# Kernel optimization log

Hardware: AMD Instinct MI355X
Metric: run time of the kernel (lower is better)

## Reference

```python
import jax, jax.numpy as jnp
import numpy as np

N, F, H, C, E = 100000, 128, 128, 40, 1600000


def setup_inputs() -> dict:
    key = jax.random.key(0)
    ks = jax.random.split(key, 8)
    x = jax.random.normal(ks[0], (N, F), dtype=jnp.float32)
    edge_index = jax.random.randint(ks[1], (2, E), 0, N, dtype=jnp.int64)
    s = 0.05
    return {
        "x": x,
        "edge_index": edge_index,
        "eps1": jnp.float32(0.0),
        "w1": jax.random.normal(ks[2], (F, H), dtype=jnp.float32) * s,
        "b1": jnp.zeros((H,), jnp.float32),
        "w2": jax.random.normal(ks[3], (H, H), dtype=jnp.float32) * s,
        "b2": jnp.zeros((H,), jnp.float32),
        "eps2": jnp.float32(0.0),
        "w3": jax.random.normal(ks[4], (H, H), dtype=jnp.float32) * s,
        "b3": jnp.zeros((H,), jnp.float32),
        "w4": jax.random.normal(ks[5], (H, C), dtype=jnp.float32) * s,
        "b4": jnp.zeros((C,), jnp.float32),
    }


def _gin_aggregate(h, src, dst, eps, n):
    # sum_{j -> i} h_j  +  (1+eps) * h_i
    agg = jax.ops.segment_sum(h[src], dst, num_segments=n)
    return (1.0 + eps) * h + agg


def reference(x, edge_index, eps1, w1, b1, w2, b2, eps2, w3, b3, w4, b4):
    src, dst = edge_index[0], edge_index[1]
    n = x.shape[0]
    # conv1: GINConv with MLP = Lin-ReLU-Lin-ReLU
    h = _gin_aggregate(x, src, dst, eps1, n)
    h = jax.nn.relu(h @ w1 + b1)
    h = jax.nn.relu(h @ w2 + b2)
    h = jax.nn.relu(h)  # outer F.relu (idempotent, kept for faithfulness)
    # dropout: identity in eval mode
    # conv2: GINConv with MLP = Lin-ReLU-Lin
    h2 = _gin_aggregate(h, src, dst, eps2, n)
    h2 = jax.nn.relu(h2 @ w3 + b3)
    h2 = h2 @ w4 + b4
    return jax.nn.log_softmax(h2, axis=1)
```

## Files before the change

kernel.cpp:

```cpp
#include <hip/hip_runtime.h>
#include <hip/hip_fp16.h>
#include <math.h>

constexpr int F = 128;
constexpr int C = 40;
constexpr int LDH = 136;
constexpr int BSHIFT = 8;
constexpr int BSIZE = 1 << BSHIFT;
constexpr int CHUNK = 8192;

typedef __attribute__((ext_vector_type(8))) _Float16 half8;
typedef __attribute__((ext_vector_type(4))) float float4v;


__global__ __launch_bounds__(256) void coarse_hist_kernel(const int* __restrict__ dst, int E, int NB,
                                                          int* __restrict__ coarse_count) {
    __shared__ int hist[512];
    int t = threadIdx.x;
    int c0 = blockIdx.x * CHUNK;
    int cend = min(c0 + CHUNK, E);
    for (int i = t; i < NB; i += 256) hist[i] = 0;
    __syncthreads();
    for (int i = c0 + t; i < cend; i += 256)
        atomicAdd(&hist[dst[i] >> BSHIFT], 1);
    __syncthreads();
    for (int i = t; i < NB; i += 256)
        if (hist[i]) atomicAdd(&coarse_count[i], hist[i]);
}

__global__ __launch_bounds__(512) void coarse_scan_kernel(const int* __restrict__ coarse_count,
                                                          int NB, int E,
                                                          int* __restrict__ coarse_start,
                                                          int* __restrict__ bucket_pos,
                                                          int* __restrict__ row_start, int N) {
    __shared__ int tmp[512];
    int t = threadIdx.x;
    int v = (t < NB) ? coarse_count[t] : 0;
    tmp[t] = v;
    __syncthreads();
    for (int d = 1; d < 512; d <<= 1) {
        int add = (t >= d) ? tmp[t - d] : 0;
        __syncthreads();
        tmp[t] += add;
        __syncthreads();
    }
    if (t < NB) {
        int ex = tmp[t] - v;
        coarse_start[t] = ex;
        bucket_pos[t] = ex;
    }
    if (t == 0) {
        coarse_start[NB] = E;
        row_start[N] = E;
    }
}

__global__ __launch_bounds__(256) void bucket_scatter_a_kernel(
        const int* __restrict__ src, const int* __restrict__ dst, int E, int NB,
        int* __restrict__ bucket_pos, unsigned* __restrict__ pairs) {
    __shared__ int hist[512];
    __shared__ int base[512];
    int t = threadIdx.x;
    int c0 = blockIdx.x * CHUNK;
    int cend = min(c0 + CHUNK, E);
    for (int i = t; i < NB; i += 256) hist[i] = 0;
    __syncthreads();
    for (int i = c0 + t; i < cend; i += 256)
        atomicAdd(&hist[dst[i] >> BSHIFT], 1);
    __syncthreads();
    for (int i = t; i < NB; i += 256) {
        int h = hist[i];
        base[i] = (h > 0) ? atomicAdd(&bucket_pos[i], h) : 0;
        hist[i] = 0;
    }
    __syncthreads();
    for (int i = c0 + t; i < cend; i += 256) {
        int d = dst[i];
        int b = d >> BSHIFT;
        int p = base[b] + atomicAdd(&hist[b], 1);
        pairs[p] = ((unsigned)(d & (BSIZE - 1)) << 24) | (unsigned)src[i];
    }
}

__global__ __launch_bounds__(256) void bucket_sort_kernel(const unsigned* __restrict__ pairs,
                                                          const int* __restrict__ coarse_start,
                                                          int N, int* __restrict__ row_start,
                                                          int* __restrict__ src_sorted) {
    __shared__ int hist[256];
    __shared__ int tmp[256];
    int b = blockIdx.x, t = threadIdx.x;
    int base = b << BSHIFT;
    int start = coarse_start[b];
    int end = coarse_start[b + 1];
    hist[t] = 0;
    __syncthreads();
    for (int i = start + t; i < end; i += 256)
        atomicAdd(&hist[pairs[i] >> 24], 1);
    __syncthreads();
    int v = hist[t];
    tmp[t] = v;
    __syncthreads();
    for (int d = 1; d < 256; d <<= 1) {
        int add = (t >= d) ? tmp[t - d] : 0;
        __syncthreads();
        tmp[t] += add;
        __syncthreads();
    }
    int ex = start + tmp[t] - v;
    if (base + t < N) row_start[base + t] = ex;
    hist[t] = ex;
    __syncthreads();
    for (int i = start + t; i < end; i += 256) {
        unsigned u = pairs[i];
        int p = atomicAdd(&hist[u >> 24], 1);
        src_sorted[p] = (int)(u & 0x00FFFFFFu);
    }
}


__global__ void conv_f16_kernel(const float* __restrict__ in, __half* __restrict__ out, int n4,
                                int* __restrict__ coarse_count, int NB) {
    int i = blockIdx.x * blockDim.x + threadIdx.x;
    if (blockIdx.x == 0) {
        for (int j = threadIdx.x; j < NB; j += 256) coarse_count[j] = 0;
    }
    if (i >= n4) return;
    float4 v = ((const float4*)in)[i];
    __half2 a = __floats2half2_rn(v.x, v.y);
    __half2 b = __floats2half2_rn(v.z, v.w);
    uint2 o;
    o.x = __builtin_bit_cast(unsigned, a);
    o.y = __builtin_bit_cast(unsigned, b);
    ((uint2*)out)[i] = o;
}


__global__ __launch_bounds__(256) void prep_weights_kernel(
        const float* __restrict__ w1, const float* __restrict__ w2,
        const float* __restrict__ w3, const float* __restrict__ w4,
        __half* __restrict__ w1t, __half* __restrict__ w2t,
        __half* __restrict__ w3t, __half* __restrict__ w4t) {
    __shared__ float lds[128 * 128];
    const float* in; __half* outp; int Nin, Npad;
    switch (blockIdx.x) {
        case 0:  in = w1; outp = w1t; Nin = 128; Npad = 128; break;
        case 1:  in = w2; outp = w2t; Nin = 128; Npad = 128; break;
        case 2:  in = w3; outp = w3t; Nin = 128; Npad = 128; break;
        default: in = w4; outp = w4t; Nin = 40;  Npad = 48;  break;
    }
    int t = threadIdx.x;
    int nf4 = 128 * Nin / 4;
    for (int i = t; i < nf4; i += 256)
        ((float4*)lds)[i] = ((const float4*)in)[i];
    __syncthreads();
    int total = Npad * 64;
    for (int i = t; i < total; i += 256) {
        int n = i >> 6, k2 = (i & 63) * 2;
        float lo = 0.f, hi = 0.f;
        if (n < Nin) {
            lo = lds[k2 * Nin + n];
            hi = lds[(k2 + 1) * Nin + n];
        }
        __half2 h = __floats2half2_rn(lo, hi);
        ((unsigned*)outp)[i] = __builtin_bit_cast(unsigned, h);
    }
}


__global__ __launch_bounds__(256) void agg_f16_kernel(const __half* __restrict__ feat,
        const int* __restrict__ row_start, const int* __restrict__ src_sorted,
        const float* __restrict__ eps_ptr, __half* __restrict__ out, int N) {
    int wid = (int)((blockIdx.x * blockDim.x + threadIdx.x) >> 6);
    int lane = threadIdx.x & 63;
    if (wid >= N) return;
    int q = lane >> 4, l16 = lane & 15;
    int s = row_start[wid], e = row_start[wid + 1];
    __half2 A0, A1, A2, A3, B0, B1, B2, B3;
    A0 = A1 = A2 = A3 = B0 = B1 = B2 = B3 = __builtin_bit_cast(__half2, 0u);
    int i = s + q;
    for (; i + 4 < e; i += 8) {
        int sv0 = src_sorted[i];
        int sv1 = src_sorted[i + 4];
        uint4 u0 = *(((const uint4*)(feat + (size_t)sv0 * F)) + l16);
        uint4 u1 = *(((const uint4*)(feat + (size_t)sv1 * F)) + l16);
        A0 = __hadd2(A0, __builtin_bit_cast(__half2, u0.x));
        A1 = __hadd2(A1, __builtin_bit_cast(__half2, u0.y));
        A2 = __hadd2(A2, __builtin_bit_cast(__half2, u0.z));
        A3 = __hadd2(A3, __builtin_bit_cast(__half2, u0.w));
        B0 = __hadd2(B0, __builtin_bit_cast(__half2, u1.x));
        B1 = __hadd2(B1, __builtin_bit_cast(__half2, u1.y));
        B2 = __hadd2(B2, __builtin_bit_cast(__half2, u1.z));
        B3 = __hadd2(B3, __builtin_bit_cast(__half2, u1.w));
    }
    if (i < e) {
        int sv = src_sorted[i];
        uint4 u = *(((const uint4*)(feat + (size_t)sv * F)) + l16);
        A0 = __hadd2(A0, __builtin_bit_cast(__half2, u.x));
        A1 = __hadd2(A1, __builtin_bit_cast(__half2, u.y));
        A2 = __hadd2(A2, __builtin_bit_cast(__half2, u.z));
        A3 = __hadd2(A3, __builtin_bit_cast(__half2, u.w));
    }
    float a[8];
    {
        float2 fa, fb;
        fa = __half22float2(A0); fb = __half22float2(B0); a[0] = fa.x + fb.x; a[1] = fa.y + fb.y;
        fa = __half22float2(A1); fb = __half22float2(B1); a[2] = fa.x + fb.x; a[3] = fa.y + fb.y;
        fa = __half22float2(A2); fb = __half22float2(B2); a[4] = fa.x + fb.x; a[5] = fa.y + fb.y;
        fa = __half22float2(A3); fb = __half22float2(B3); a[6] = fa.x + fb.x; a[7] = fa.y + fb.y;
    }
#pragma unroll
    for (int j = 0; j < 8; ++j) {
        a[j] += __shfl_xor(a[j], 16);
        a[j] += __shfl_xor(a[j], 32);
    }
    if (q == 0) {
        float ep1 = 1.0f + *eps_ptr;
        uint4 u = *(((const uint4*)(feat + (size_t)wid * F)) + l16);
        float2 s0 = __half22float2(__builtin_bit_cast(__half2, u.x));
        float2 s1 = __half22float2(__builtin_bit_cast(__half2, u.y));
        float2 s2 = __half22float2(__builtin_bit_cast(__half2, u.z));
        float2 s3 = __half22float2(__builtin_bit_cast(__half2, u.w));
        a[0] = fmaf(ep1, s0.x, a[0]); a[1] = fmaf(ep1, s0.y, a[1]);
        a[2] = fmaf(ep1, s1.x, a[2]); a[3] = fmaf(ep1, s1.y, a[3]);
        a[4] = fmaf(ep1, s2.x, a[4]); a[5] = fmaf(ep1, s2.y, a[5]);
        a[6] = fmaf(ep1, s3.x, a[6]); a[7] = fmaf(ep1, s3.y, a[7]);
        uint4 ou;
        ou.x = __builtin_bit_cast(unsigned, __floats2half2_rn(a[0], a[1]));
        ou.y = __builtin_bit_cast(unsigned, __floats2half2_rn(a[2], a[3]));
        ou.z = __builtin_bit_cast(unsigned, __floats2half2_rn(a[4], a[5]));
        ou.w = __builtin_bit_cast(unsigned, __floats2half2_rn(a[6], a[7]));
        *(((uint4*)(out + (size_t)wid * F)) + l16) = ou;
    }
}


__global__ __launch_bounds__(256) void mlp1_mfma_kernel(const __half* __restrict__ A,
        const __half* __restrict__ w1t, const float* __restrict__ b1,
        const __half* __restrict__ w2t, const float* __restrict__ b2,
        __half* __restrict__ out, int N) {
    __shared__ __half ldsA[64 * LDH];
    __shared__ __half ldsW[128 * LDH];
    __shared__ float ldsB[256];
    int t = threadIdx.x;
    int wave = t >> 6, lane = t & 63, quad = lane >> 4, l16 = lane & 15;
    int br = blockIdx.x * 64;
    if (t < 128) ldsB[t] = b1[t];
    else         ldsB[t] = b2[t - 128];
    for (int i = t; i < 1024; i += 256) {
        int r = i >> 4, c = i & 15;
        int gr = br + r;
        uint4 v = make_uint4(0u, 0u, 0u, 0u);
        if (gr < N) v = *((const uint4*)(A + (size_t)gr * F + c * 8));
        *((uint4*)&ldsA[r * LDH + c * 8]) = v;
    }
    for (int i = t; i < 2048; i += 256) {
        int r = i >> 4, c = i & 15;
        *((uint4*)&ldsW[r * LDH + c * 8]) = *((const uint4*)(w1t + r * 128 + c * 8));
    }
    __syncthreads();

    int ct0 = wave * 2;
    float4v acc[4][2];
    float4v zero = {0.f, 0.f, 0.f, 0.f};
#pragma unroll
    for (int i = 0; i < 4; ++i)
#pragma unroll
        for (int j = 0; j < 2; ++j) acc[i][j] = zero;

#pragma unroll
    for (int ks = 0; ks < 4; ++ks) {
        half8 af[4], wf[2];
#pragma unroll
        for (int i = 0; i < 4; ++i)
            af[i] = *((const half8*)&ldsA[(i * 16 + l16) * LDH + ks * 32 + quad * 8]);
#pragma unroll
        for (int j = 0; j < 2; ++j)
            wf[j] = *((const half8*)&ldsW[((ct0 + j) * 16 + l16) * LDH + ks * 32 + quad * 8]);
#pragma unroll
        for (int i = 0; i < 4; ++i)
#pragma unroll
            for (int j = 0; j < 2; ++j)
                acc[i][j] = __builtin_amdgcn_mfma_f32_16x16x32_f16(wf[j], af[i], acc[i][j], 0, 0, 0);
    }
    __syncthreads();
#pragma unroll
    for (int j = 0; j < 2; ++j) {
        int c = ct0 + j;
        float4 bb = *((const float4*)&ldsB[c * 16 + quad * 4]);
#pragma unroll
        for (int i = 0; i < 4; ++i) {
            float v0 = acc[i][j][0] + bb.x; v0 = v0 > 0.f ? v0 : 0.f;
            float v1 = acc[i][j][1] + bb.y; v1 = v1 > 0.f ? v1 : 0.f;
            float v2 = acc[i][j][2] + bb.z; v2 = v2 > 0.f ? v2 : 0.f;
            float v3 = acc[i][j][3] + bb.w; v3 = v3 > 0.f ? v3 : 0.f;
            __half2 h0 = __floats2half2_rn(v0, v1);
            __half2 h1 = __floats2half2_rn(v2, v3);
            uint2 o;
            o.x = __builtin_bit_cast(unsigned, h0);
            o.y = __builtin_bit_cast(unsigned, h1);
            *((uint2*)&ldsA[(i * 16 + l16) * LDH + c * 16 + quad * 4]) = o;
        }
    }
    for (int i = t; i < 2048; i += 256) {
        int r = i >> 4, c = i & 15;
        *((uint4*)&ldsW[r * LDH + c * 8]) = *((const uint4*)(w2t + r * 128 + c * 8));
    }
    __syncthreads();

#pragma unroll
    for (int i = 0; i < 4; ++i)
#pragma unroll
        for (int j = 0; j < 2; ++j) acc[i][j] = zero;
#pragma unroll
    for (int ks = 0; ks < 4; ++ks) {
        half8 af[4], wf[2];
#pragma unroll
        for (int i = 0; i < 4; ++i)
            af[i] = *((const half8*)&ldsA[(i * 16 + l16) * LDH + ks * 32 + quad * 8]);
#pragma unroll
        for (int j = 0; j < 2; ++j)
            wf[j] = *((const half8*)&ldsW[((ct0 + j) * 16 + l16) * LDH + ks * 32 + quad * 8]);
#pragma unroll
        for (int i = 0; i < 4; ++i)
#pragma unroll
            for (int j = 0; j < 2; ++j)
                acc[i][j] = __builtin_amdgcn_mfma_f32_16x16x32_f16(wf[j], af[i], acc[i][j], 0, 0, 0);
    }
    __syncthreads();
#pragma unroll
    for (int j = 0; j < 2; ++j) {
        int c = ct0 + j;
        float4 bb = *((const float4*)&ldsB[128 + c * 16 + quad * 4]);
#pragma unroll
        for (int i = 0; i < 4; ++i) {
            float v0 = acc[i][j][0] + bb.x; v0 = v0 > 0.f ? v0 : 0.f;
            float v1 = acc[i][j][1] + bb.y; v1 = v1 > 0.f ? v1 : 0.f;
            float v2 = acc[i][j][2] + bb.z; v2 = v2 > 0.f ? v2 : 0.f;
            float v3 = acc[i][j][3] + bb.w; v3 = v3 > 0.f ? v3 : 0.f;
            __half2 h0 = __floats2half2_rn(v0, v1);
            __half2 h1 = __floats2half2_rn(v2, v3);
            uint2 o;
            o.x = __builtin_bit_cast(unsigned, h0);
            o.y = __builtin_bit_cast(unsigned, h1);
            *((uint2*)&ldsA[(i * 16 + l16) * LDH + c * 16 + quad * 4]) = o;
        }
    }
    __syncthreads();
    for (int i = t; i < 1024; i += 256) {
        int r = i >> 4, c = i & 15;
        int gr = br + r;
        if (gr < N)
            *((uint4*)(out + (size_t)gr * F + c * 8)) = *((const uint4*)&ldsA[r * LDH + c * 8]);
    }
}


__global__ __launch_bounds__(256) void mlp2_mfma_kernel(const __half* __restrict__ A,
        const __half* __restrict__ w3t, const float* __restrict__ b3,
        const __half* __restrict__ w4t, const float* __restrict__ b4,
        float* __restrict__ out, int N) {
    __shared__ __half ldsA[64 * LDH];
    __shared__ __half ldsW[128 * LDH];
    __shared__ float ldsB[176];
    int t = threadIdx.x;
    int wave = t >> 6, lane = t & 63, quad = lane >> 4, l16 = lane & 15;
    int br = blockIdx.x * 64;
    if (t < 128) ldsB[t] = b3[t];
    else if (t < 176) ldsB[t] = (t - 128 < C) ? b4[t - 128] : 0.f;
    for (int i = t; i < 1024; i += 256) {
        int r = i >> 4, c = i & 15;
        int gr = br + r;
        uint4 v = make_uint4(0u, 0u, 0u, 0u);
        if (gr < N) v = *((const uint4*)(A + (size_t)gr * F + c * 8));
        *((uint4*)&ldsA[r * LDH + c * 8]) = v;
    }
    for (int i = t; i < 2048; i += 256) {
        int r = i >> 4, c = i & 15;
        *((uint4*)&ldsW[r * LDH + c * 8]) = *((const uint4*)(w3t + r * 128 + c * 8));
    }
    __syncthreads();

    int ct0 = wave * 2;
    float4v acc[4][2];
    float4v zero = {0.f, 0.f, 0.f, 0.f};
#pragma unroll
    for (int i = 0; i < 4; ++i)
#pragma unroll
        for (int j = 0; j < 2; ++j) acc[i][j] = zero;
#pragma unroll
    for (int ks = 0; ks < 4; ++ks) {
        half8 af[4], wf[2];
#pragma unroll
        for (int i = 0; i < 4; ++i)
            af[i] = *((const half8*)&ldsA[(i * 16 + l16) * LDH + ks * 32 + quad * 8]);
#pragma unroll
        for (int j = 0; j < 2; ++j)
            wf[j] = *((const half8*)&ldsW[((ct0 + j) * 16 + l16) * LDH + ks * 32 + quad * 8]);
#pragma unroll
        for (int i = 0; i < 4; ++i)
#pragma unroll
            for (int j = 0; j < 2; ++j)
                acc[i][j] = __builtin_amdgcn_mfma_f32_16x16x32_f16(wf[j], af[i], acc[i][j], 0, 0, 0);
    }
    __syncthreads();
#pragma unroll
    for (int j = 0; j < 2; ++j) {
        int c = ct0 + j;
        float4 bb = *((const float4*)&ldsB[c * 16 + quad * 4]);
#pragma unroll
        for (int i = 0; i < 4; ++i) {
            float v0 = acc[i][j][0] + bb.x; v0 = v0 > 0.f ? v0 : 0.f;
            float v1 = acc[i][j][1] + bb.y; v1 = v1 > 0.f ? v1 : 0.f;
            float v2 = acc[i][j][2] + bb.z; v2 = v2 > 0.f ? v2 : 0.f;
            float v3 = acc[i][j][3] + bb.w; v3 = v3 > 0.f ? v3 : 0.f;
            __half2 h0 = __floats2half2_rn(v0, v1);
            __half2 h1 = __floats2half2_rn(v2, v3);
            uint2 o;
            o.x = __builtin_bit_cast(unsigned, h0);
            o.y = __builtin_bit_cast(unsigned, h1);
            *((uint2*)&ldsA[(i * 16 + l16) * LDH + c * 16 + quad * 4]) = o;
        }
    }
    for (int i = t; i < 768; i += 256) {
        int r = i >> 4, c = i & 15;
        *((uint4*)&ldsW[r * LDH + c * 8]) = *((const uint4*)(w4t + r * 128 + c * 8));
    }
    __syncthreads();

    float4v acc4[3];
#pragma unroll
    for (int c = 0; c < 3; ++c) acc4[c] = zero;
#pragma unroll
    for (int ks = 0; ks < 4; ++ks) {
        half8 af = *((const half8*)&ldsA[(wave * 16 + l16) * LDH + ks * 32 + quad * 8]);
#pragma unroll
        for (int c = 0; c < 3; ++c) {
            half8 wf = *((const half8*)&ldsW[(c * 16 + l16) * LDH + ks * 32 + quad * 8]);
            acc4[c] = __builtin_amdgcn_mfma_f32_16x16x32_f16(wf, af, acc4[c], 0, 0, 0);
        }
    }
    float lv[3][4];
#pragma unroll
    for (int c = 0; c < 3; ++c) {
        float4 bb = *((const float4*)&ldsB[128 + c * 16 + quad * 4]);
        lv[c][0] = acc4[c][0] + bb.x;
        lv[c][1] = acc4[c][1] + bb.y;
        lv[c][2] = acc4[c][2] + bb.z;
        lv[c][3] = acc4[c][3] + bb.w;
    }
    bool tile2ok = (quad < 2);
    float m = -1e30f;
#pragma unroll
    for (int c = 0; c < 3; ++c) {
        if (c == 2 && !tile2ok) continue;
#pragma unroll
        for (int r = 0; r < 4; ++r) m = fmaxf(m, lv[c][r]);
    }
    m = fmaxf(m, __shfl_xor(m, 16));
    m = fmaxf(m, __shfl_xor(m, 32));
    float ssum = 0.f;
#pragma unroll
    for (int c = 0; c < 3; ++c) {
        if (c == 2 && !tile2ok) continue;
#pragma unroll
        for (int r = 0; r < 4; ++r) ssum += __expf(lv[c][r] - m);
    }
    ssum += __shfl_xor(ssum, 16);
    ssum += __shfl_xor(ssum, 32);
    float L = m + __logf(ssum);
    int node = br + wave * 16 + l16;
    if (node < N) {
#pragma unroll
        for (int c = 0; c < 3; ++c) {
            if (c == 2 && !tile2ok) continue;
            float4 o = make_float4(lv[c][0] - L, lv[c][1] - L, lv[c][2] - L, lv[c][3] - L);
            *((float4*)(out + (size_t)node * C + c * 16 + quad * 4)) = o;
        }
    }
}


extern "C" void kernel_launch(void* const* d_in, const int* in_sizes, int n_in,
                              void* d_out, int out_size, void* d_ws, size_t ws_size,
                              hipStream_t stream) {
    const float* x    = (const float*)d_in[0];
    const int*   ei   = (const int*)d_in[1];
    const float* eps1 = (const float*)d_in[2];
    const float* w1   = (const float*)d_in[3];
    const float* b1   = (const float*)d_in[4];
    const float* w2   = (const float*)d_in[5];
    const float* b2   = (const float*)d_in[6];
    const float* eps2 = (const float*)d_in[7];
    const float* w3   = (const float*)d_in[8];
    const float* b3   = (const float*)d_in[9];
    const float* w4   = (const float*)d_in[10];
    const float* b4   = (const float*)d_in[11];
    float* out = (float*)d_out;

    int N = in_sizes[0] / F;
    int E = in_sizes[1] / 2;
    const int* src = ei;
    const int* dst = ei + E;

    int NB = (N + BSIZE - 1) >> BSHIFT;
    int BA = (E + CHUNK - 1) / CHUNK;

    __half* x_h  = (__half*)d_ws;
    __half* h0_h = x_h + (size_t)N * F;
    __half* h_h  = h0_h + (size_t)N * F;
    __half* w1t  = h_h + (size_t)N * F;
    __half* w2t  = w1t + 128 * 128;
    __half* w3t  = w2t + 128 * 128;
    __half* w4t  = w3t + 128 * 128;
    unsigned* pairs   = (unsigned*)(w4t + 48 * 128);
    int* row_start    = (int*)(pairs + E);
    int* src_sorted   = row_start + (N + 1);
    int* coarse_count = src_sorted + E;
    int* coarse_start = coarse_count + 512;
    int* bucket_pos   = coarse_start + 513;

    int n4 = N * F / 4;
    conv_f16_kernel<<<(n4 + 255) / 256, 256, 0, stream>>>(x, x_h, n4, coarse_count, NB);
    prep_weights_kernel<<<4, 256, 0, stream>>>(w1, w2, w3, w4, w1t, w2t, w3t, w4t);

    coarse_hist_kernel<<<BA, 256, 0, stream>>>(dst, E, NB, coarse_count);
    coarse_scan_kernel<<<1, 512, 0, stream>>>(coarse_count, NB, E, coarse_start, bucket_pos,
                                              row_start, N);
    bucket_scatter_a_kernel<<<BA, 256, 0, stream>>>(src, dst, E, NB, bucket_pos, pairs);
    bucket_sort_kernel<<<NB, 256, 0, stream>>>(pairs, coarse_start, N, row_start, src_sorted);

    agg_f16_kernel<<<(N + 3) / 4, 256, 0, stream>>>(x_h, row_start, src_sorted, eps1, h0_h, N);
    mlp1_mfma_kernel<<<(N + 63) / 64, 256, 0, stream>>>(h0_h, w1t, b1, w2t, b2, h_h, N);
    agg_f16_kernel<<<(N + 3) / 4, 256, 0, stream>>>(h_h, row_start, src_sorted, eps2, h0_h, N);
    mlp2_mfma_kernel<<<(N + 63) / 64, 256, 0, stream>>>(h0_h, w3t, b3, w4t, b4, out, N);
}
```

Baseline: 352.0 us.

## Fuse prep kernels and process two nodes per wave in aggregation

The histogram, weight transpose and x-to-fp16 conversion kernels are merged into one launch, and a memset now zeroes the coarse counts. The aggregation kernel now gives each wave two destination nodes, loads up to 16 neighbor indices per node in one coalesced read, spreads them with shuffles, and issues eight feature gathers per iteration. This cuts launch count and raises memory-level parallelism in the gather. In exchange it adds masked redundant loads for low-degree nodes and more register pressure, and the weight transpose now runs in four passes through a smaller LDS buffer.

New measurement: 344.4 us. -2.2%, faster.

```diff
diff --git a/kernel.cpp b/kernel.cpp
--- a/kernel.cpp
+++ b/kernel.cpp
@@ -13,20 +13,66 @@
 typedef __attribute__((ext_vector_type(4))) float float4v;
 
 
-__global__ __launch_bounds__(256) void coarse_hist_kernel(const int* __restrict__ dst, int E, int NB,
-                                                          int* __restrict__ coarse_count) {
-    __shared__ int hist[512];
-    int t = threadIdx.x;
-    int c0 = blockIdx.x * CHUNK;
-    int cend = min(c0 + CHUNK, E);
-    for (int i = t; i < NB; i += 256) hist[i] = 0;
-    __syncthreads();
-    for (int i = c0 + t; i < cend; i += 256)
-        atomicAdd(&hist[dst[i] >> BSHIFT], 1);
-    __syncthreads();
-    for (int i = t; i < NB; i += 256)
-        if (hist[i]) atomicAdd(&coarse_count[i], hist[i]);
-}
+__global__ __launch_bounds__(256) void fused_prep_kernel(
+        const float* __restrict__ x, __half* __restrict__ x_h, int n4,
+        const int* __restrict__ dst, int E, int NB, int* __restrict__ coarse_count,
+        const float* __restrict__ w1, const float* __restrict__ w2,
+        const float* __restrict__ w3, const float* __restrict__ w4,
+        __half* __restrict__ w1t, __half* __restrict__ w2t,
+        __half* __restrict__ w3t, __half* __restrict__ w4t, int BA) {
+    __shared__ float smem[4096];
+    int b = blockIdx.x, t = threadIdx.x;
+    if (b < BA) {
+        int* hist = (int*)smem;
+        int c0 = b * CHUNK, cend = min(c0 + CHUNK, E);
+        for (int i = t; i < NB; i += 256) hist[i] = 0;
+        __syncthreads();
+        for (int i = c0 + t; i < cend; i += 256)
+            atomicAdd(&hist[dst[i] >> BSHIFT], 1);
+        __syncthreads();
+        for (int i = t; i < NB; i += 256)
+            if (hist[i]) atomicAdd(&coarse_count[i], hist[i]);
+        return;
+    }
+    if (b < BA + 4) {
+        const float* in; __half* outp; int Nin, Npad;
+        switch (b - BA) {
+            case 0:  in = w1; outp = w1t; Nin = 128; Npad = 128; break;
+            case 1:  in = w2; outp = w2t; Nin = 128; Npad = 128; break;
+            case 2:  in = w3; outp = w3t; Nin = 128; Npad = 128; break;
+            default: in = w4; outp = w4t; Nin = 40;  Npad = 48;  break;
+        }
+        for (int p = 0; p < 4; ++p) {
+            int nf4 = 32 * Nin / 4;
+            const float4* srcv = (const float4*)(in + 32 * p * Nin);
+            for (int i = t; i < nf4; i += 256) ((float4*)smem)[i] = srcv[i];
+            __syncthreads();
+            int total = Npad * 16;
+            for (int i = t; i < total; i += 256) {
+                int n = i >> 4, wl = i & 15;
+                float lo = 0.f, hi = 0.f;
+                if (n < Nin) {
+                    lo = smem[(2 * wl) * Nin + n];
+                    hi = smem[(2 * wl + 1) * Nin + n];
+                }
+                __half2 h = __floats2half2_rn(lo, hi);
+                ((unsigned*)outp)[n * 64 + 16 * p + wl] = __builtin_bit_cast(unsigned, h);
+            }
+            __syncthreads();
+        }
+        return;
+    }
+    int i = (b - BA - 4) * 256 + t;
+    if (i >= n4) return;
+    float4 v = ((const float4*)x)[i];
+    __half2 a = __floats2half2_rn(v.x, v.y);
+    __half2 bb = __floats2half2_rn(v.z, v.w);
+    uint2 o;
+    o.x = __builtin_bit_cast(unsigned, a);
+    o.y = __builtin_bit_cast(unsigned, bb);
+    ((uint2*)x_h)[i] = o;
+}
+
 
 __global__ __launch_bounds__(512) void coarse_scan_kernel(const int* __restrict__ coarse_count,
                                                           int NB, int E,
@@ -118,118 +164,140 @@
 }
 
 
-__global__ void conv_f16_kernel(const float* __restrict__ in, __half* __restrict__ out, int n4,
-                                int* __restrict__ coarse_count, int NB) {
-    int i = blockIdx.x * blockDim.x + threadIdx.x;
-    if (blockIdx.x == 0) {
-        for (int j = threadIdx.x; j < NB; j += 256) coarse_count[j] = 0;
-    }
-    if (i >= n4) return;
-    float4 v = ((const float4*)in)[i];
-    __half2 a = __floats2half2_rn(v.x, v.y);
-    __half2 b = __floats2half2_rn(v.z, v.w);
-    uint2 o;
-    o.x = __builtin_bit_cast(unsigned, a);
-    o.y = __builtin_bit_cast(unsigned, b);
-    ((uint2*)out)[i] = o;
-}
-
-
-__global__ __launch_bounds__(256) void prep_weights_kernel(
-        const float* __restrict__ w1, const float* __restrict__ w2,
-        const float* __restrict__ w3, const float* __restrict__ w4,
-        __half* __restrict__ w1t, __half* __restrict__ w2t,
-        __half* __restrict__ w3t, __half* __restrict__ w4t) {
-    __shared__ float lds[128 * 128];
-    const float* in; __half* outp; int Nin, Npad;
-    switch (blockIdx.x) {
-        case 0:  in = w1; outp = w1t; Nin = 128; Npad = 128; break;
-        case 1:  in = w2; outp = w2t; Nin = 128; Npad = 128; break;
-        case 2:  in = w3; outp = w3t; Nin = 128; Npad = 128; break;
-        default: in = w4; outp = w4t; Nin = 40;  Npad = 48;  break;
-    }
-    int t = threadIdx.x;
-    int nf4 = 128 * Nin / 4;
-    for (int i = t; i < nf4; i += 256)
-        ((float4*)lds)[i] = ((const float4*)in)[i];
-    __syncthreads();
-    int total = Npad * 64;
-    for (int i = t; i < total; i += 256) {
-        int n = i >> 6, k2 = (i & 63) * 2;
-        float lo = 0.f, hi = 0.f;
-        if (n < Nin) {
-            lo = lds[k2 * Nin + n];
-            hi = lds[(k2 + 1) * Nin + n];
-        }
-        __half2 h = __floats2half2_rn(lo, hi);
-        ((unsigned*)outp)[i] = __builtin_bit_cast(unsigned, h);
-    }
-}
-
-
 __global__ __launch_bounds__(256) void agg_f16_kernel(const __half* __restrict__ feat,
         const int* __restrict__ row_start, const int* __restrict__ src_sorted,
         const float* __restrict__ eps_ptr, __half* __restrict__ out, int N) {
-    int wid = (int)((blockIdx.x * blockDim.x + threadIdx.x) >> 6);
+    int wp = (int)((blockIdx.x * blockDim.x + threadIdx.x) >> 6);
     int lane = threadIdx.x & 63;
-    if (wid >= N) return;
+    int n0 = wp * 2;
+    if (n0 >= N) return;
     int q = lane >> 4, l16 = lane & 15;
-    int s = row_start[wid], e = row_start[wid + 1];
-    __half2 A0, A1, A2, A3, B0, B1, B2, B3;
-    A0 = A1 = A2 = A3 = B0 = B1 = B2 = B3 = __builtin_bit_cast(__half2, 0u);
-    int i = s + q;
-    for (; i + 4 < e; i += 8) {
-        int sv0 = src_sorted[i];
-        int sv1 = src_sorted[i + 4];
-        uint4 u0 = *(((const uint4*)(feat + (size_t)sv0 * F)) + l16);
-        uint4 u1 = *(((const uint4*)(feat + (size_t)sv1 * F)) + l16);
-        A0 = __hadd2(A0, __builtin_bit_cast(__half2, u0.x));
-        A1 = __hadd2(A1, __builtin_bit_cast(__half2, u0.y));
-        A2 = __hadd2(A2, __builtin_bit_cast(__half2, u0.z));
-        A3 = __hadd2(A3, __builtin_bit_cast(__half2, u0.w));
-        B0 = __hadd2(B0, __builtin_bit_cast(__half2, u1.x));
-        B1 = __hadd2(B1, __builtin_bit_cast(__half2, u1.y));
-        B2 = __hadd2(B2, __builtin_bit_cast(__half2, u1.z));
-        B3 = __hadd2(B3, __builtin_bit_cast(__half2, u1.w));
-    }
-    if (i < e) {
-        int sv = src_sorted[i];
-        uint4 u = *(((const uint4*)(feat + (size_t)sv * F)) + l16);
-        A0 = __hadd2(A0, __builtin_bit_cast(__half2, u.x));
-        A1 = __hadd2(A1, __builtin_bit_cast(__half2, u.y));
-        A2 = __hadd2(A2, __builtin_bit_cast(__half2, u.z));
-        A3 = __hadd2(A3, __builtin_bit_cast(__half2, u.w));
-    }
-    float a[8];
+    bool has1 = (n0 + 1) < N;
+    int s0 = row_start[n0];
+    int e0 = row_start[n0 + 1];
+    int s1 = e0;
+    int e1 = has1 ? row_start[n0 + 2] : e0;
+    uint4 self0 = *(((const uint4*)(feat + (size_t)n0 * F)) + l16);
+    uint4 self1 = has1 ? *(((const uint4*)(feat + (size_t)(n0 + 1) * F)) + l16)
+                       : make_uint4(0u, 0u, 0u, 0u);
+    float ep1 = 1.0f + *eps_ptr;
+    __half2 PA0, PA1, PA2, PA3, PB0, PB1, PB2, PB3;
+    __half2 QA0, QA1, QA2, QA3, QB0, QB1, QB2, QB3;
+    PA0 = PA1 = PA2 = PA3 = PB0 = PB1 = PB2 = PB3 = __builtin_bit_cast(__half2, 0u);
+    QA0 = QA1 = QA2 = QA3 = QB0 = QB1 = QB2 = QB3 = __builtin_bit_cast(__half2, 0u);
+    const uint4 z4 = make_uint4(0u, 0u, 0u, 0u);
+    int i0 = s0, i1 = s1;
+    while (i0 < e0 || i1 < e1) {
+        int svA = src_sorted[max(min(i0 + l16, e0 - 1), 0)];
+        int svB = src_sorted[max(min(i1 + l16, e1 - 1), 0)];
+        int a0 = __shfl(svA, q);
+        int a1 = __shfl(svA, q + 4);
+        int a2 = __shfl(svA, q + 8);
+        int a3 = __shfl(svA, q + 12);
+        int b0 = __shfl(svB, q);
+        int b1 = __shfl(svB, q + 4);
+        int b2 = __shfl(svB, q + 8);
+        int b3 = __shfl(svB, q + 12);
+        uint4 uA0 = *(((const uint4*)(feat + (size_t)a0 * F)) + l16);
+        uint4 uA1 = *(((const uint4*)(feat + (size_t)a1 * F)) + l16);
+        uint4 uA2 = *(((const uint4*)(feat + (size_t)a2 * F)) + l16);
+        uint4 uA3 = *(((const uint4*)(feat + (size_t)a3 * F)) + l16);
+        uint4 uB0 = *(((const uint4*)(feat + (size_t)b0 * F)) + l16);
+        uint4 uB1 = *(((const uint4*)(feat + (size_t)b1 * F)) + l16);
+        uint4 uB2 = *(((const uint4*)(feat + (size_t)b2 * F)) + l16);
+        uint4 uB3 = *(((const uint4*)(feat + (size_t)b3 * F)) + l16);
+        if (i0 + q >= e0)      uA0 = z4;
+        if (i0 + q + 4 >= e0)  uA1 = z4;
+        if (i0 + q + 8 >= e0)  uA2 = z4;
+        if (i0 + q + 12 >= e0) uA3 = z4;
+        if (i1 + q >= e1)      uB0 = z4;
+        if (i1 + q + 4 >= e1)  uB1 = z4;
+        if (i1 + q + 8 >= e1)  uB2 = z4;
+        if (i1 + q + 12 >= e1) uB3 = z4;
+        PA0 = __hadd2(PA0, __builtin_bit_cast(__half2, uA0.x));
+        PA1 = __hadd2(PA1, __builtin_bit_cast(__half2, uA0.y));
+        PA2 = __hadd2(PA2, __builtin_bit_cast(__half2, uA0.z));
+        PA3 = __hadd2(PA3, __builtin_bit_cast(__half2, uA0.w));
+        PB0 = __hadd2(PB0, __builtin_bit_cast(__half2, uA1.x));
+        PB1 = __hadd2(PB1, __builtin_bit_cast(__half2, uA1.y));
+        PB2 = __hadd2(PB2, __builtin_bit_cast(__half2, uA1.z));
+        PB3 = __hadd2(PB3, __builtin_bit_cast(__half2, uA1.w));
+        PA0 = __hadd2(PA0, __builtin_bit_cast(__half2, uA2.x));
+        PA1 = __hadd2(PA1, __builtin_bit_cast(__half2, uA2.y));
+        PA2 = __hadd2(PA2, __builtin_bit_cast(__half2, uA2.z));
+        PA3 = __hadd2(PA3, __builtin_bit_cast(__half2, uA2.w));
+        PB0 = __hadd2(PB0, __builtin_bit_cast(__half2, uA3.x));
+        PB1 = __hadd2(PB1, __builtin_bit_cast(__half2, uA3.y));
+        PB2 = __hadd2(PB2, __builtin_bit_cast(__half2, uA3.z));
+        PB3 = __hadd2(PB3, __builtin_bit_cast(__half2, uA3.w));
+        QA0 = __hadd2(QA0, __builtin_bit_cast(__half2, uB0.x));
+        QA1 = __hadd2(QA1, __builtin_bit_cast(__half2, uB0.y));
+        QA2 = __hadd2(QA2, __builtin_bit_cast(__half2, uB0.z));
+        QA3 = __hadd2(QA3, __builtin_bit_cast(__half2, uB0.w));
+        QB0 = __hadd2(QB0, __builtin_bit_cast(__half2, uB1.x));
+        QB1 = __hadd2(QB1, __builtin_bit_cast(__half2, uB1.y));
+        QB2 = __hadd2(QB2, __builtin_bit_cast(__half2, uB1.z));
+        QB3 = __hadd2(QB3, __builtin_bit_cast(__half2, uB1.w));
+        QA0 = __hadd2(QA0, __builtin_bit_cast(__half2, uB2.x));
+        QA1 = __hadd2(QA1, __builtin_bit_cast(__half2, uB2.y));
+        QA2 = __hadd2(QA2, __builtin_bit_cast(__half2, uB2.z));
+        QA3 = __hadd2(QA3, __builtin_bit_cast(__half2, uB2.w));
+        QB0 = __hadd2(QB0, __builtin_bit_cast(__half2, uB3.x));
+        QB1 = __hadd2(QB1, __builtin_bit_cast(__half2, uB3.y));
+        QB2 = __hadd2(QB2, __builtin_bit_cast(__half2, uB3.z));
+        QB3 = __hadd2(QB3, __builtin_bit_cast(__half2, uB3.w));
+        i0 += 16;
+        i1 += 16;
+    }
+    float a[8], c[8];
     {
         float2 fa, fb;
-        fa = __half22float2(A0); fb = __half22float2(B0); a[0] = fa.x + fb.x; a[1] = fa.y + fb.y;
-        fa = __half22float2(A1); fb = __half22float2(B1); a[2] = fa.x + fb.x; a[3] = fa.y + fb.y;
-        fa = __half22float2(A2); fb = __half22float2(B2); a[4] = fa.x + fb.x; a[5] = fa.y + fb.y;
-        fa = __half22float2(A3); fb = __half22float2(B3); a[6] = fa.x + fb.x; a[7] = fa.y + fb.y;
+        fa = __half22float2(PA0); fb = __half22float2(PB0); a[0] = fa.x + fb.x; a[1] = fa.y + fb.y;
+        fa = __half22float2(PA1); fb = __half22float2(PB1); a[2] = fa.x + fb.x; a[3] = fa.y + fb.y;
+        fa = __half22float2(PA2); fb = __half22float2(PB2); a[4] = fa.x + fb.x; a[5] = fa.y + fb.y;
+        fa = __half22float2(PA3); fb = __half22float2(PB3); a[6] = fa.x + fb.x; a[7] = fa.y + fb.y;
+        fa = __half22float2(QA0); fb = __half22float2(QB0); c[0] = fa.x + fb.x; c[1] = fa.y + fb.y;
+        fa = __half22float2(QA1); fb = __half22float2(QB1); c[2] = fa.x + fb.x; c[3] = fa.y + fb.y;
+        fa = __half22float2(QA2); fb = __half22float2(QB2); c[4] = fa.x + fb.x; c[5] = fa.y + fb.y;
+        fa = __half22float2(QA3); fb = __half22float2(QB3); c[6] = fa.x + fb.x; c[7] = fa.y + fb.y;
     }
 #pragma unroll
     for (int j = 0; j < 8; ++j) {
         a[j] += __shfl_xor(a[j], 16);
         a[j] += __shfl_xor(a[j], 32);
+        c[j] += __shfl_xor(c[j], 16);
+        c[j] += __shfl_xor(c[j], 32);
     }
     if (q == 0) {
-        float ep1 = 1.0f + *eps_ptr;
-        uint4 u = *(((const uint4*)(feat + (size_t)wid * F)) + l16);
-        float2 s0 = __half22float2(__builtin_bit_cast(__half2, u.x));
-        float2 s1 = __half22float2(__builtin_bit_cast(__half2, u.y));
-        float2 s2 = __half22float2(__builtin_bit_cast(__half2, u.z));
-        float2 s3 = __half22float2(__builtin_bit_cast(__half2, u.w));
-        a[0] = fmaf(ep1, s0.x, a[0]); a[1] = fmaf(ep1, s0.y, a[1]);
-        a[2] = fmaf(ep1, s1.x, a[2]); a[3] = fmaf(ep1, s1.y, a[3]);
-        a[4] = fmaf(ep1, s2.x, a[4]); a[5] = fmaf(ep1, s2.y, a[5]);
-        a[6] = fmaf(ep1, s3.x, a[6]); a[7] = fmaf(ep1, s3.y, a[7]);
+        float2 s0f = __half22float2(__builtin_bit_cast(__half2, self0.x));
+        float2 s1f = __half22float2(__builtin_bit_cast(__half2, self0.y));
+        float2 s2f = __half22float2(__builtin_bit_cast(__half2, self0.z));
+        float2 s3f = __half22float2(__builtin_bit_cast(__half2, self0.w));
+        a[0] = fmaf(ep1, s0f.x, a[0]); a[1] = fmaf(ep1, s0f.y, a[1]);
+        a[2] = fmaf(ep1, s1f.x, a[2]); a[3] = fmaf(ep1, s1f.y, a[3]);
+        a[4] = fmaf(ep1, s2f.x, a[4]); a[5] = fmaf(ep1, s2f.y, a[5]);
+        a[6] = fmaf(ep1, s3f.x, a[6]); a[7] = fmaf(ep1, s3f.y, a[7]);
         uint4 ou;
         ou.x = __builtin_bit_cast(unsigned, __floats2half2_rn(a[0], a[1]));
         ou.y = __builtin_bit_cast(unsigned, __floats2half2_rn(a[2], a[3]));
         ou.z = __builtin_bit_cast(unsigned, __floats2half2_rn(a[4], a[5]));
         ou.w = __builtin_bit_cast(unsigned, __floats2half2_rn(a[6], a[7]));
-        *(((uint4*)(out + (size_t)wid * F)) + l16) = ou;
+        *(((uint4*)(out + (size_t)n0 * F)) + l16) = ou;
+    } else if (q == 1 && has1) {
+        float2 s0f = __half22float2(__builtin_bit_cast(__half2, self1.x));
+        float2 s1f = __half22float2(__builtin_bit_cast(__half2, self1.y));
+        float2 s2f = __half22float2(__builtin_bit_cast(__half2, self1.z));
+        float2 s3f = __half22float2(__builtin_bit_cast(__half2, self1.w));
+        c[0] = fmaf(ep1, s0f.x, c[0]); c[1] = fmaf(ep1, s0f.y, c[1]);
+        c[2] = fmaf(ep1, s1f.x, c[2]); c[3] = fmaf(ep1, s1f.y, c[3]);
+        c[4] = fmaf(ep1, s2f.x, c[4]); c[5] = fmaf(ep1, s2f.y, c[5]);
+        c[6] = fmaf(ep1, s3f.x, c[6]); c[7] = fmaf(ep1, s3f.y, c[7]);
+        uint4 ou;
+        ou.x = __builtin_bit_cast(unsigned, __floats2half2_rn(c[0], c[1]));
+        ou.y = __builtin_bit_cast(unsigned, __floats2half2_rn(c[2], c[3]));
+        ou.z = __builtin_bit_cast(unsigned, __floats2half2_rn(c[4], c[5]));
+        ou.w = __builtin_bit_cast(unsigned, __floats2half2_rn(c[6], c[7]));
+        *(((uint4*)(out + (size_t)(n0 + 1) * F)) + l16) = ou;
     }
 }
 
@@ -520,17 +588,21 @@
     int* bucket_pos   = coarse_start + 513;
 
     int n4 = N * F / 4;
-    conv_f16_kernel<<<(n4 + 255) / 256, 256, 0, stream>>>(x, x_h, n4, coarse_count, NB);
-    prep_weights_kernel<<<4, 256, 0, stream>>>(w1, w2, w3, w4, w1t, w2t, w3t, w4t);
-
-    coarse_hist_kernel<<<BA, 256, 0, stream>>>(dst, E, NB, coarse_count);
+    int NCONV = (n4 + 255) / 256;
+
+    hipMemsetAsync(coarse_count, 0, 512 * sizeof(int), stream);
+    fused_prep_kernel<<<BA + 4 + NCONV, 256, 0, stream>>>(x, x_h, n4, dst, E, NB, coarse_count,
+                                                          w1, w2, w3, w4, w1t, w2t, w3t, w4t, BA);
+
     coarse_scan_kernel<<<1, 512, 0, stream>>>(coarse_count, NB, E, coarse_start, bucket_pos,
                                               row_start, N);
     bucket_scatter_a_kernel<<<BA, 256, 0, stream>>>(src, dst, E, NB, bucket_pos, pairs);
     bucket_sort_kernel<<<NB, 256, 0, stream>>>(pairs, coarse_start, N, row_start, src_sorted);
 
-    agg_f16_kernel<<<(N + 3) / 4, 256, 0, stream>>>(x_h, row_start, src_sorted, eps1, h0_h, N);
+    int nwp = (N + 1) / 2;
+    int aggblocks = (nwp + 3) / 4;
+    agg_f16_kernel<<<aggblocks, 256, 0, stream>>>(x_h, row_start, src_sorted, eps1, h0_h, N);
     mlp1_mfma_kernel<<<(N + 63) / 64, 256, 0, stream>>>(h0_h, w1t, b1, w2t, b2, h_h, N);
-    agg_f16_kernel<<<(N + 3) / 4, 256, 0, stream>>>(h_h, row_start, src_sorted, eps2, h0_h, N);
+    agg_f16_kernel<<<aggblocks, 256, 0, stream>>>(h_h, row_start, src_sorted, eps2, h0_h, N);
     mlp2_mfma_kernel<<<(N + 63) / 64, 256, 0, stream>>>(h0_h, w3t, b3, w4t, b4, out, N);
 }
```

## Store features in column slices for cache-local gather and fuse prep kernels

Applied to the files above, without the earlier changes.

Features are now stored as eight 16-column slices, each contiguous across nodes. Each aggregation block processes one slice, so a slice's gather working set (100k × 32 B) can stay resident in cache. Within a wave, each group of 4 lanes handles one edge, and 16 edges are processed at a time. The histogram, weight transpose and x conversion now run in one fused launch, with a memset replacing the in-kernel zeroing. In exchange, the edge lists and row pointers are read eight times instead of once, and each gather moves only 8 bytes per lane.

New measurement: 550.6 us. +56.4%, slower.

```diff
diff --git a/kernel.cpp b/kernel.cpp
--- a/kernel.cpp
+++ b/kernel.cpp
@@ -8,25 +8,72 @@
 constexpr int BSHIFT = 8;
 constexpr int BSIZE = 1 << BSHIFT;
 constexpr int CHUNK = 8192;
+constexpr int NSLICE = 8;
+constexpr int SLICE_H = 16;
 
 typedef __attribute__((ext_vector_type(8))) _Float16 half8;
 typedef __attribute__((ext_vector_type(4))) float float4v;
 
 
-__global__ __launch_bounds__(256) void coarse_hist_kernel(const int* __restrict__ dst, int E, int NB,
-                                                          int* __restrict__ coarse_count) {
-    __shared__ int hist[512];
-    int t = threadIdx.x;
-    int c0 = blockIdx.x * CHUNK;
-    int cend = min(c0 + CHUNK, E);
-    for (int i = t; i < NB; i += 256) hist[i] = 0;
-    __syncthreads();
-    for (int i = c0 + t; i < cend; i += 256)
-        atomicAdd(&hist[dst[i] >> BSHIFT], 1);
-    __syncthreads();
-    for (int i = t; i < NB; i += 256)
-        if (hist[i]) atomicAdd(&coarse_count[i], hist[i]);
-}
+__global__ __launch_bounds__(256) void fused_prep_kernel(
+        const float* __restrict__ x, __half* __restrict__ x_sl, int N, int n32,
+        const int* __restrict__ dst, int E, int NB, int* __restrict__ coarse_count,
+        const float* __restrict__ w1, const float* __restrict__ w2,
+        const float* __restrict__ w3, const float* __restrict__ w4,
+        __half* __restrict__ w1t, __half* __restrict__ w2t,
+        __half* __restrict__ w3t, __half* __restrict__ w4t, int BA) {
+    __shared__ float smem[4096];
+    int b = blockIdx.x, t = threadIdx.x;
+    if (b < BA) {
+        int* hist = (int*)smem;
+        int c0 = b * CHUNK, cend = min(c0 + CHUNK, E);
+        for (int i = t; i < NB; i += 256) hist[i] = 0;
+        __syncthreads();
+        for (int i = c0 + t; i < cend; i += 256)
+            atomicAdd(&hist[dst[i] >> BSHIFT], 1);
+        __syncthreads();
+        for (int i = t; i < NB; i += 256)
+            if (hist[i]) atomicAdd(&coarse_count[i], hist[i]);
+        return;
+    }
+    if (b < BA + 4) {
+        const float* in; __half* outp; int Nin, Npad;
+        switch (b - BA) {
+            case 0:  in = w1; outp = w1t; Nin = 128; Npad = 128; break;
+            case 1:  in = w2; outp = w2t; Nin = 128; Npad = 128; break;
+            case 2:  in = w3; outp = w3t; Nin = 128; Npad = 128; break;
+            default: in = w4; outp = w4t; Nin = 40;  Npad = 48;  break;
+        }
+        for (int p = 0; p < 4; ++p) {
+            int nf4 = 32 * Nin / 4;
+            const float4* srcv = (const float4*)(in + 32 * p * Nin);
+            for (int i = t; i < nf4; i += 256) ((float4*)smem)[i] = srcv[i];
+            __syncthreads();
+            int total = Npad * 16;
+            for (int i = t; i < total; i += 256) {
+                int n = i >> 4, wl = i & 15;
+                float lo = 0.f, hi = 0.f;
+                if (n < Nin) {
+                    lo = smem[(2 * wl) * Nin + n];
+                    hi = smem[(2 * wl + 1) * Nin + n];
+                }
+                __half2 h = __floats2half2_rn(lo, hi);
+                ((unsigned*)outp)[n * 64 + 16 * p + wl] = __builtin_bit_cast(unsigned, h);
+            }
+            __syncthreads();
+        }
+        return;
+    }
+    int j = (b - BA - 4) * 256 + t;
+    if (j >= n32) return;
+    int n = j >> 5, q = j & 31, s = q >> 2, r = q & 3;
+    float4 v = *((const float4*)(x + (size_t)n * F + s * SLICE_H + r * 4));
+    uint2 o;
+    o.x = __builtin_bit_cast(unsigned, __floats2half2_rn(v.x, v.y));
+    o.y = __builtin_bit_cast(unsigned, __floats2half2_rn(v.z, v.w));
+    *((uint2*)(x_sl + (size_t)s * N * SLICE_H + (size_t)n * SLICE_H + r * 4)) = o;
+}
+
 
 __global__ __launch_bounds__(512) void coarse_scan_kernel(const int* __restrict__ coarse_count,
                                                           int NB, int E,
@@ -118,118 +165,68 @@
 }
 
 
-__global__ void conv_f16_kernel(const float* __restrict__ in, __half* __restrict__ out, int n4,
-                                int* __restrict__ coarse_count, int NB) {
-    int i = blockIdx.x * blockDim.x + threadIdx.x;
-    if (blockIdx.x == 0) {
-        for (int j = threadIdx.x; j < NB; j += 256) coarse_count[j] = 0;
-    }
-    if (i >= n4) return;
-    float4 v = ((const float4*)in)[i];
-    __half2 a = __floats2half2_rn(v.x, v.y);
-    __half2 b = __floats2half2_rn(v.z, v.w);
-    uint2 o;
-    o.x = __builtin_bit_cast(unsigned, a);
-    o.y = __builtin_bit_cast(unsigned, b);
-    ((uint2*)out)[i] = o;
-}
-
-
-__global__ __launch_bounds__(256) void prep_weights_kernel(
-        const float* __restrict__ w1, const float* __restrict__ w2,
-        const float* __restrict__ w3, const float* __restrict__ w4,
-        __half* __restrict__ w1t, __half* __restrict__ w2t,
-        __half* __restrict__ w3t, __half* __restrict__ w4t) {
-    __shared__ float lds[128 * 128];
-    const float* in; __half* outp; int Nin, Npad;
-    switch (blockIdx.x) {
-        case 0:  in = w1; outp = w1t; Nin = 128; Npad = 128; break;
-        case 1:  in = w2; outp = w2t; Nin = 128; Npad = 128; break;
-        case 2:  in = w3; outp = w3t; Nin = 128; Npad = 128; break;
-        default: in = w4; outp = w4t; Nin = 40;  Npad = 48;  break;
-    }
-    int t = threadIdx.x;
-    int nf4 = 128 * Nin / 4;
-    for (int i = t; i < nf4; i += 256)
-        ((float4*)lds)[i] = ((const float4*)in)[i];
-    __syncthreads();
-    int total = Npad * 64;
-    for (int i = t; i < total; i += 256) {
-        int n = i >> 6, k2 = (i & 63) * 2;
-        float lo = 0.f, hi = 0.f;
-        if (n < Nin) {
-            lo = lds[k2 * Nin + n];
-            hi = lds[(k2 + 1) * Nin + n];
-        }
-        __half2 h = __floats2half2_rn(lo, hi);
-        ((unsigned*)outp)[i] = __builtin_bit_cast(unsigned, h);
-    }
-}
-
-
-__global__ __launch_bounds__(256) void agg_f16_kernel(const __half* __restrict__ feat,
+__global__ __launch_bounds__(256) void agg_slice_kernel(const __half* __restrict__ feat_sl,
         const int* __restrict__ row_start, const int* __restrict__ src_sorted,
         const float* __restrict__ eps_ptr, __half* __restrict__ out, int N) {
-    int wid = (int)((blockIdx.x * blockDim.x + threadIdx.x) >> 6);
-    int lane = threadIdx.x & 63;
-    if (wid >= N) return;
-    int q = lane >> 4, l16 = lane & 15;
-    int s = row_start[wid], e = row_start[wid + 1];
-    __half2 A0, A1, A2, A3, B0, B1, B2, B3;
-    A0 = A1 = A2 = A3 = B0 = B1 = B2 = B3 = __builtin_bit_cast(__half2, 0u);
-    int i = s + q;
-    for (; i + 4 < e; i += 8) {
-        int sv0 = src_sorted[i];
-        int sv1 = src_sorted[i + 4];
-        uint4 u0 = *(((const uint4*)(feat + (size_t)sv0 * F)) + l16);
-        uint4 u1 = *(((const uint4*)(feat + (size_t)sv1 * F)) + l16);
-        A0 = __hadd2(A0, __builtin_bit_cast(__half2, u0.x));
-        A1 = __hadd2(A1, __builtin_bit_cast(__half2, u0.y));
-        A2 = __hadd2(A2, __builtin_bit_cast(__half2, u0.z));
-        A3 = __hadd2(A3, __builtin_bit_cast(__half2, u0.w));
-        B0 = __hadd2(B0, __builtin_bit_cast(__half2, u1.x));
-        B1 = __hadd2(B1, __builtin_bit_cast(__half2, u1.y));
-        B2 = __hadd2(B2, __builtin_bit_cast(__half2, u1.z));
-        B3 = __hadd2(B3, __builtin_bit_cast(__half2, u1.w));
-    }
-    if (i < e) {
-        int sv = src_sorted[i];
-        uint4 u = *(((const uint4*)(feat + (size_t)sv * F)) + l16);
-        A0 = __hadd2(A0, __builtin_bit_cast(__half2, u.x));
-        A1 = __hadd2(A1, __builtin_bit_cast(__half2, u.y));
-        A2 = __hadd2(A2, __builtin_bit_cast(__half2, u.z));
-        A3 = __hadd2(A3, __builtin_bit_cast(__half2, u.w));
-    }
-    float a[8];
-    {
-        float2 fa, fb;
-        fa = __half22float2(A0); fb = __half22float2(B0); a[0] = fa.x + fb.x; a[1] = fa.y + fb.y;
-        fa = __half22float2(A1); fb = __half22float2(B1); a[2] = fa.x + fb.x; a[3] = fa.y + fb.y;
-        fa = __half22float2(A2); fb = __half22float2(B2); a[4] = fa.x + fb.x; a[5] = fa.y + fb.y;
-        fa = __half22float2(A3); fb = __half22float2(B3); a[6] = fa.x + fb.x; a[7] = fa.y + fb.y;
-    }
-#pragma unroll
-    for (int j = 0; j < 8; ++j) {
-        a[j] += __shfl_xor(a[j], 16);
-        a[j] += __shfl_xor(a[j], 32);
-    }
-    if (q == 0) {
-        float ep1 = 1.0f + *eps_ptr;
-        uint4 u = *(((const uint4*)(feat + (size_t)wid * F)) + l16);
-        float2 s0 = __half22float2(__builtin_bit_cast(__half2, u.x));
-        float2 s1 = __half22float2(__builtin_bit_cast(__half2, u.y));
-        float2 s2 = __half22float2(__builtin_bit_cast(__half2, u.z));
-        float2 s3 = __half22float2(__builtin_bit_cast(__half2, u.w));
-        a[0] = fmaf(ep1, s0.x, a[0]); a[1] = fmaf(ep1, s0.y, a[1]);
-        a[2] = fmaf(ep1, s1.x, a[2]); a[3] = fmaf(ep1, s1.y, a[3]);
-        a[4] = fmaf(ep1, s2.x, a[4]); a[5] = fmaf(ep1, s2.y, a[5]);
-        a[6] = fmaf(ep1, s3.x, a[6]); a[7] = fmaf(ep1, s3.y, a[7]);
-        uint4 ou;
-        ou.x = __builtin_bit_cast(unsigned, __floats2half2_rn(a[0], a[1]));
-        ou.y = __builtin_bit_cast(unsigned, __floats2half2_rn(a[2], a[3]));
-        ou.z = __builtin_bit_cast(unsigned, __floats2half2_rn(a[4], a[5]));
-        ou.w = __builtin_bit_cast(unsigned, __floats2half2_rn(a[6], a[7]));
-        *(((uint4*)(out + (size_t)wid * F)) + l16) = ou;
+    int t = threadIdx.x;
+    int wave = t >> 6, lane = t & 63;
+    int g = lane >> 2, r = lane & 3;
+    int slice = blockIdx.x & 7;
+    int n0 = (int)(blockIdx.x >> 3) * 16 + wave * 4;
+    if (n0 >= N) return;
+    const uint2* sb = (const uint2*)(feat_sl + (size_t)slice * N * SLICE_H);
+    float ep1 = 1.0f + *eps_ptr;
+    for (int k = 0; k < 4; ++k) {
+        int n = n0 + k;
+        if (n >= N) break;
+        int s = row_start[n], e = row_start[n + 1];
+        uint2 su = sb[(size_t)n * 4 + r];
+        __half2 a0, a1, b0, b1;
+        a0 = a1 = b0 = b1 = __builtin_bit_cast(__half2, 0u);
+        int i = s;
+        for (; i + 16 < e; i += 32) {
+            int iB = i + 16 + g;
+            int svA = src_sorted[i + g];
+            int svB = src_sorted[iB < e ? iB : (e - 1)];
+            uint2 uA = sb[(size_t)svA * 4 + r];
+            uint2 uB = sb[(size_t)svB * 4 + r];
+            if (iB >= e) { uB.x = 0u; uB.y = 0u; }
+            a0 = __hadd2(a0, __builtin_bit_cast(__half2, uA.x));
+            a1 = __hadd2(a1, __builtin_bit_cast(__half2, uA.y));
+            b0 = __hadd2(b0, __builtin_bit_cast(__half2, uB.x));
+            b1 = __hadd2(b1, __builtin_bit_cast(__half2, uB.y));
+        }
+        if (i < e) {
+            int iA = i + g;
+            int svA = src_sorted[iA < e ? iA : (e - 1)];
+            uint2 uA = sb[(size_t)svA * 4 + r];
+            if (iA >= e) { uA.x = 0u; uA.y = 0u; }
+            a0 = __hadd2(a0, __builtin_bit_cast(__half2, uA.x));
+            a1 = __hadd2(a1, __builtin_bit_cast(__half2, uA.y));
+        }
+        float2 fa0 = __half22float2(a0), fb0 = __half22float2(b0);
+        float2 fa1 = __half22float2(a1), fb1 = __half22float2(b1);
+        float v0 = fa0.x + fb0.x, v1 = fa0.y + fb0.y;
+        float v2 = fa1.x + fb1.x, v3 = fa1.y + fb1.y;
+#pragma unroll
+        for (int m = 4; m <= 32; m <<= 1) {
+            v0 += __shfl_xor(v0, m);
+            v1 += __shfl_xor(v1, m);
+            v2 += __shfl_xor(v2, m);
+            v3 += __shfl_xor(v3, m);
+        }
+        if (g == 0) {
+            float2 s0 = __half22float2(__builtin_bit_cast(__half2, su.x));
+            float2 s1 = __half22float2(__builtin_bit_cast(__half2, su.y));
+            v0 = fmaf(ep1, s0.x, v0);
+            v1 = fmaf(ep1, s0.y, v1);
+            v2 = fmaf(ep1, s1.x, v2);
+            v3 = fmaf(ep1, s1.y, v3);
+            uint2 ou;
+            ou.x = __builtin_bit_cast(unsigned, __floats2half2_rn(v0, v1));
+            ou.y = __builtin_bit_cast(unsigned, __floats2half2_rn(v2, v3));
+            *((uint2*)(out + (size_t)n * F + slice * SLICE_H + r * 4)) = ou;
+        }
     }
 }
 
@@ -237,7 +234,7 @@
 __global__ __launch_bounds__(256) void mlp1_mfma_kernel(const __half* __restrict__ A,
         const __half* __restrict__ w1t, const float* __restrict__ b1,
         const __half* __restrict__ w2t, const float* __restrict__ b2,
-        __half* __restrict__ out, int N) {
+        __half* __restrict__ out_sl, int N) {
     __shared__ __half ldsA[64 * LDH];
     __shared__ __half ldsW[128 * LDH];
     __shared__ float ldsB[256];
@@ -349,8 +346,11 @@
     for (int i = t; i < 1024; i += 256) {
         int r = i >> 4, c = i & 15;
         int gr = br + r;
-        if (gr < N)
-            *((uint4*)(out + (size_t)gr * F + c * 8)) = *((const uint4*)&ldsA[r * LDH + c * 8]);
+        if (gr < N) {
+            int s = c >> 1, p = c & 1;
+            *((uint4*)(out_sl + (size_t)s * N * SLICE_H + (size_t)gr * SLICE_H + p * 8)) =
+                *((const uint4*)&ldsA[r * LDH + c * 8]);
+        }
     }
 }
 
@@ -505,10 +505,10 @@
     int NB = (N + BSIZE - 1) >> BSHIFT;
     int BA = (E + CHUNK - 1) / CHUNK;
 
-    __half* x_h  = (__half*)d_ws;
-    __half* h0_h = x_h + (size_t)N * F;
-    __half* h_h  = h0_h + (size_t)N * F;
-    __half* w1t  = h_h + (size_t)N * F;
+    __half* x_sl = (__half*)d_ws;
+    __half* h0_h = x_sl + (size_t)N * F;
+    __half* h_sl = h0_h + (size_t)N * F;
+    __half* w1t  = h_sl + (size_t)N * F;
     __half* w2t  = w1t + 128 * 128;
     __half* w3t  = w2t + 128 * 128;
     __half* w4t  = w3t + 128 * 128;
@@ -519,18 +519,24 @@
     int* coarse_start = coarse_count + 512;
     int* bucket_pos   = coarse_start + 513;
 
-    int n4 = N * F / 4;
-    conv_f16_kernel<<<(n4 + 255) / 256, 256, 0, stream>>>(x, x_h, n4, coarse_count, NB);
-    prep_weights_kernel<<<4, 256, 0, stream>>>(w1, w2, w3, w4, w1t, w2t, w3t, w4t);
-
-    coarse_hist_kernel<<<BA, 256, 0, stream>>>(dst, E, NB, coarse_count);
+    int n32 = N * 32;
+    int NCONV = (n32 + 255) / 256;
+
+    hipMemsetAsync(coarse_count, 0, 512 * sizeof(int), stream);
+    fused_prep_kernel<<<BA + 4 + NCONV, 256, 0, stream>>>(x, x_sl, N, n32, dst, E, NB,
+                                                          coarse_count, w1, w2, w3, w4,
+                                                          w1t, w2t, w3t, w4t, BA);
+
     coarse_scan_kernel<<<1, 512, 0, stream>>>(coarse_count, NB, E, coarse_start, bucket_pos,
                                               row_start, N);
     bucket_scatter_a_kernel<<<BA, 256, 0, stream>>>(src, dst, E, NB, bucket_pos, pairs);
     bucket_sort_kernel<<<NB, 256, 0, stream>>>(pairs, coarse_start, N, row_start, src_sorted);
 
-    agg_f16_kernel<<<(N + 3) / 4, 256, 0, stream>>>(x_h, row_start, src_sorted, eps1, h0_h, N);
-    mlp1_mfma_kernel<<<(N + 63) / 64, 256, 0, stream>>>(h0_h, w1t, b1, w2t, b2, h_h, N);
-    agg_f16_kernel<<<(N + 3) / 4, 256, 0, stream>>>(h_h, row_start, src_sorted, eps2, h0_h, N);
+    int NBLK = (N + 15) / 16;
+    agg_slice_kernel<<<NBLK * NSLICE, 256, 0, stream>>>(x_sl, row_start, src_sorted, eps1,
+                                                        h0_h, N);
+    mlp1_mfma_kernel<<<(N + 63) / 64, 256, 0, stream>>>(h0_h, w1t, b1, w2t, b2, h_sl, N);
+    agg_slice_kernel<<<NBLK * NSLICE, 256, 0, stream>>>(h_sl, row_start, src_sorted, eps2,
+                                                        h0_h, N);
     mlp2_mfma_kernel<<<(N + 63) / 64, 256, 0, stream>>>(h0_h, w3t, b3, w4t, b4, out, N);
 }
```
